# Optimization experiments

Measured on AMD Instinct MI355X. Metric: run time of the kernel, lower is better.

## Reference

```python
import jax, jax.numpy as jnp
import numpy as np

GRID_N = 3   # number of grid intervals (pykan 'grid')
K = 3        # spline order (pykan 'k')
IN_F = 512
OUT_F = 512
BATCH = 8
SEQ = 2048


def _extended_grid(d, dtype):
    # base grid: num+1 points over [-1, 1]; extend by K steps of h on each side (pykan extend_grid)
    pts = jnp.linspace(-1.0, 1.0, GRID_N + 1).astype(dtype)
    h = jnp.asarray(2.0 / GRID_N, dtype)
    left = pts[0] + h * jnp.arange(-K, 0, dtype=dtype)
    right = pts[-1] + h * jnp.arange(1, K + 1, dtype=dtype)
    ext = jnp.concatenate([left, pts, right])           # (GRID_N + 1 + 2K,)
    return jnp.broadcast_to(ext, (d, ext.shape[0]))     # per-input-feature grid (shared values)


def _bspline_basis(x, grid):
    # Cox-de Boor recursion, vectorized over tokens and input features.
    # x: (N, D), grid: (D, M) -> returns (N, D, M-1-K) = (N, D, GRID_N+K)
    x = x[:, :, None]                     # (N, D, 1)
    g = grid[None, :, :]                  # (1, D, M)
    B = ((x >= g[..., :-1]) & (x < g[..., 1:])).astype(x.dtype)
    for p in range(1, K + 1):
        left = (x - g[..., :-(p + 1)]) / (g[..., p:-1] - g[..., :-(p + 1)])
        right = (g[..., p + 1:] - x) / (g[..., p + 1:] - g[..., 1:-p])
        B = left * B[..., :-1] + right * B[..., 1:]
    return B


def setup_inputs() -> dict:
    key = jax.random.key(0)
    k1, k2, k3 = jax.random.split(key, 3)
    x = jax.random.normal(k1, (BATCH, SEQ, IN_F), dtype=jnp.float32)
    coef = jax.random.normal(k2, (OUT_F, IN_F, GRID_N + K), dtype=jnp.float32) * 0.1
    scale_base = (1.0 / np.sqrt(IN_F)) + (jax.random.uniform(k3, (OUT_F, IN_F), dtype=jnp.float32) * 2.0 - 1.0) * 0.1
    scale_sp = jnp.ones((OUT_F, IN_F), dtype=jnp.float32)
    bias = jnp.zeros((OUT_F,), dtype=jnp.float32)
    return {"x": x, "coef": coef, "scale_base": scale_base, "scale_sp": scale_sp, "bias": bias}


def reference(x, coef, scale_base, scale_sp, bias):
    B_, S, D = x.shape
    xf = x.reshape(-1, D)                               # (N, D) tokens
    grid = _extended_grid(D, xf.dtype)
    basis = _bspline_basis(xf, grid)                    # (N, D, GRID_N+K)
    base = jax.nn.silu(xf)                              # base activation per input feature
    # per-edge: scale_base*silu(x_i) + scale_sp*spline(x_i); sum over input features, add bias
    spline_w = scale_sp[..., None] * coef               # (O, D, GRID_N+K)
    y = (jnp.einsum('ni,oi->no', base, scale_base)
         + jnp.einsum('nib,oib->no', basis, spline_w)
         + bias[None, :])
    return y.reshape(B_, S, -1)
```

## Files before the change

kernel.cpp:

```cpp
#include <hip/hip_runtime.h>


typedef short        bf16x8 __attribute__((ext_vector_type(8)));
typedef float        f32x4  __attribute__((ext_vector_type(4)));
typedef unsigned int u32x4  __attribute__((ext_vector_type(4)));

#define NROWS 16384
#define DIN   512
#define DOUT  512
#define BM    64
#define BN    512
#define NKT   64

__device__ __forceinline__ unsigned short f2bf(float f) {
    unsigned int u = __float_as_uint(f);
    u += 0x7fffu + ((u >> 16) & 1u);
    return (unsigned short)(u >> 16);
}

__device__ __forceinline__ void kan_act_store(float xv, char* p16) {
    float S  = __builtin_fmaf(xv, 1.5f, 4.5f);
    float jf = floorf(S);
    float t  = S - jf;
    int   j  = (int)jf;
    float t2 = t * t;
    float t3 = t2 * t;
    float omt  = 1.0f - t;
    float omt2 = omt * omt;
    float n0 = omt2 * omt * (1.0f / 6.0f);
    float n1 = __builtin_fmaf(t3, 0.5f, -t2) + (2.0f / 3.0f);
    float u  = (t + t2) - t3;
    float n2 = __builtin_fmaf(u, 0.5f, 1.0f / 6.0f);
    float n3 = t3 * (1.0f / 6.0f);
    float e  = __expf(-xv);
    float si = xv * __builtin_amdgcn_rcpf(1.0f + e);

    unsigned P01, P23, WS;
    asm("v_cvt_pk_bf16_f32 %0, %1, %2" : "=v"(P01) : "v"(n0), "v"(n1));
    asm("v_cvt_pk_bf16_f32 %0, %1, %2" : "=v"(P23) : "v"(n2), "v"(n3));
    asm("v_cvt_pk_bf16_f32 %0, %1, %2" : "=v"(WS)  : "v"(si), "v"(0.0f));
    unsigned U = P01 << 16;
    unsigned V = (P01 >> 16) | (P23 << 16);
    unsigned Z = P23 >> 16;
    bool odd = (j & 1) != 0;
    unsigned c0 = odd ? U : P01;
    unsigned c1 = odd ? V : P23;
    unsigned c2 = odd ? Z : 0u;
    int b = (j - 2) >> 1;
    u32x4 w;
    w[0] = (b == 0) ? c0 : (b == -1) ? c1 : (b == -2) ? c2 : 0u;
    w[1] = (b == 1) ? c0 : (b ==  0) ? c1 : (b == -1) ? c2 : 0u;
    w[2] = (b == 2) ? c0 : (b ==  1) ? c1 : (b ==  0) ? c2 : 0u;
    w[3] = (b == 3) ? c0 : (b ==  2) ? c1 : (b ==  1) ? c2 : 0u;
    w[0] = (w[0] & 0xFFFF0000u) | (WS & 0xFFFFu);
    *(u32x4*)p16 = w;
}

__global__ __launch_bounds__(256) void kan_prep(
    const float* __restrict__ coef, const float* __restrict__ scale_base,
    const float* __restrict__ scale_sp, unsigned short* __restrict__ wt)
{
    int t = blockIdx.x * 256 + threadIdx.x;
    int o = t >> 9;
    int i = t & 511;
    float sb = scale_base[t];
    float sp = scale_sp[t];
    const float* cp = coef + (size_t)t * 6;
    bf16x8 w;
    w[0] = (short)f2bf(sb);
#pragma unroll
    for (int b = 0; b < 6; ++b) w[1 + b] = (short)f2bf(sp * cp[b]);
    w[7] = 0;
    int kt = i >> 3, s = i & 7, ks = s >> 2, fg = s & 3;
    size_t off = ((size_t)((kt * 2 + ks) * 512 + o)) * 64 + fg * 16;
    *(bf16x8*)((char*)wt + off) = w;
}

__global__ __launch_bounds__(512, 2) void kan_gemm(
    const float* __restrict__ x, const unsigned short* __restrict__ wt,
    const float* __restrict__ bias, float* __restrict__ y)
{
    __shared__ char As[2][BM * 128];

    const int tid  = threadIdx.x;
    const int lane = tid & 63;
    const int wid  = tid >> 6;

    int bid = blockIdx.x;
    int mt  = (bid & 7) * 32 + (bid >> 3);

    const int row0 = mt * BM;

    const int ar = tid >> 3;
    const int ap = tid & 7;
    const float* xp = x + (size_t)(row0 + ar) * DIN + ap;
    const int as_sw = (ar & 7) << 4;
    const int c0 = ap << 4;
    char* const arow0 = &As[0][ar * 128];
    char* const arow1 = &As[1][ar * 128];

    const int fr = lane & 15;
    const int fg = lane >> 4;

    const char* wb = (const char*)wt;
    int colpart[4];
#pragma unroll
    for (int n2 = 0; n2 < 4; ++n2)
        colpart[n2] = (wid * 64 + n2 * 16 + fr) * 64 + fg * 16;

#define LOADB(B, ktv)                                                         \
    {                                                                         \
        _Pragma("unroll")                                                     \
        for (int q = 0; q < 8; ++q) {                                         \
            int n2_ = q & 3, ks_ = q >> 2;                                    \
            B[q] = *(const bf16x8*)(wb + (size_t)((ktv) * 2 + ks_) * 32768    \
                                    + colpart[n2_]);                          \
        }                                                                     \
    }

    f32x4 acc[4][4];
#pragma unroll
    for (int m2 = 0; m2 < 4; ++m2)
#pragma unroll
        for (int n2 = 0; n2 < 4; ++n2) {
            f32x4 z = {0.f, 0.f, 0.f, 0.f};
            acc[m2][n2] = z;
        }

    bf16x8 Ba[8], Bb[8];

    LOADB(Ba, 0);
    kan_act_store(xp[0], arow0 + (c0 ^ as_sw));
    float xb = xp[8];
    asm volatile("s_waitcnt lgkmcnt(0)" ::: "memory");
    __builtin_amdgcn_s_barrier();

#define STEP(ktv, Bcur, Bnext)                                                \
    {                                                                         \
        const int cur_ = (ktv) & 1;                                           \
        bf16x8 af_[2][4];                                                     \
        _Pragma("unroll")                                                     \
        for (int ks_ = 0; ks_ < 2; ++ks_) {                                   \
            _Pragma("unroll")                                                 \
            for (int m2_ = 0; m2_ < 4; ++m2_) {                               \
                int rr_ = m2_ * 16 + fr;                                      \
                af_[ks_][m2_] = *(const bf16x8*)(&As[cur_][0] + rr_ * 128     \
                    + ((ks_ * 64 + fg * 16) ^ ((rr_ & 7) << 4)));             \
            }                                                                 \
        }                                                                     \
        if ((ktv) + 1 < NKT) {                                                \
            LOADB(Bnext, (ktv) + 1);                                          \
            char* rowp_ = (((ktv) + 1) & 1) ? arow1 : arow0;                  \
            kan_act_store(xb, rowp_ + (c0 ^ as_sw));                          \
            if ((ktv) + 2 < NKT) xb = xp[((ktv) + 2) * 8];                    \
        }                                                                     \
        __builtin_amdgcn_s_setprio(1);                                        \
        _Pragma("unroll")                                                     \
        for (int ks_ = 0; ks_ < 2; ++ks_)                                     \
            _Pragma("unroll")                                                 \
            for (int m2_ = 0; m2_ < 4; ++m2_)                                 \
                _Pragma("unroll")                                             \
                for (int n2_ = 0; n2_ < 4; ++n2_)                             \
                    acc[m2_][n2_] = __builtin_amdgcn_mfma_f32_16x16x32_bf16(  \
                        af_[ks_][m2_], Bcur[ks_ * 4 + n2_], acc[m2_][n2_],    \
                        0, 0, 0);                                             \
        __builtin_amdgcn_s_setprio(0);                                        \
        asm volatile("s_waitcnt lgkmcnt(0)" ::: "memory");                    \
        __builtin_amdgcn_s_barrier();                                         \
    }

    for (int kt = 0; kt < NKT; kt += 2) {
        STEP(kt, Ba, Bb);
        STEP(kt + 1, Bb, Ba);
    }

    const int orow0 = row0 + fg * 4;
    const int ocol0 = wid * 64 + fr;
#pragma unroll
    for (int n2 = 0; n2 < 4; ++n2) {
        float bv = bias[ocol0 + n2 * 16];
#pragma unroll
        for (int m2 = 0; m2 < 4; ++m2) {
#pragma unroll
            for (int r = 0; r < 4; ++r) {
                y[(size_t)(orow0 + m2 * 16 + r) * DOUT + (ocol0 + n2 * 16)]
                    = acc[m2][n2][r] + bv;
            }
        }
    }
#undef STEP
#undef LOADB
}

extern "C" void kernel_launch(void* const* d_in, const int* in_sizes, int n_in,
                              void* d_out, int out_size, void* d_ws, size_t ws_size,
                              hipStream_t stream)
{
    const float* x          = (const float*)d_in[0];
    const float* coef       = (const float*)d_in[1];
    const float* scale_base = (const float*)d_in[2];
    const float* scale_sp   = (const float*)d_in[3];
    const float* bias       = (const float*)d_in[4];
    unsigned short* wt = (unsigned short*)d_ws;
    float* y = (float*)d_out;

    kan_prep<<<1024, 256, 0, stream>>>(coef, scale_base, scale_sp, wt);
    kan_gemm<<<256, 512, 0, stream>>>(x, wt, bias, y);
}
```

Measured before the change: 91.01 us.

## Split GEMM block into MFMA consumer waves and activation producer waves

Adds four producer waves per block that compute the SiLU and cubic B-spline basis values and write them into the double-buffered LDS tile. The eight original waves now only load weights and issue MFMAs. The goal is to take the transcendental and basis arithmetic off the MFMA waves' critical path. In exchange the block grows to 768 threads with a tighter launch-bounds occupancy hint, which may restrict register allocation and cause spills of the accumulator tiles.

```diff
diff --git a/kernel.cpp b/kernel.cpp
--- a/kernel.cpp
+++ b/kernel.cpp
@@ -76,7 +76,7 @@
     *(bf16x8*)((char*)wt + off) = w;
 }
 
-__global__ __launch_bounds__(512, 2) void kan_gemm(
+__global__ __launch_bounds__(768, 3) void kan_gemm(
     const float* __restrict__ x, const unsigned short* __restrict__ wt,
     const float* __restrict__ bias, float* __restrict__ y)
 {
@@ -88,25 +88,17 @@
 
     int bid = blockIdx.x;
     int mt  = (bid & 7) * 32 + (bid >> 3);
-
     const int row0 = mt * BM;
-
-    const int ar = tid >> 3;
-    const int ap = tid & 7;
-    const float* xp = x + (size_t)(row0 + ar) * DIN + ap;
-    const int as_sw = (ar & 7) << 4;
-    const int c0 = ap << 4;
-    char* const arow0 = &As[0][ar * 128];
-    char* const arow1 = &As[1][ar * 128];
 
     const int fr = lane & 15;
     const int fg = lane >> 4;
 
-    const char* wb = (const char*)wt;
-    int colpart[4];
-#pragma unroll
-    for (int n2 = 0; n2 < 4; ++n2)
-        colpart[n2] = (wid * 64 + n2 * 16 + fr) * 64 + fg * 16;
+    if (wid < 8) {
+        const char* wb = (const char*)wt;
+        int colpart[4];
+#pragma unroll
+        for (int n2 = 0; n2 < 4; ++n2)
+            colpart[n2] = (wid * 64 + n2 * 16 + fr) * 64 + fg * 16;
 
 #define LOADB(B, ktv)                                                         \
     {                                                                         \
@@ -118,24 +110,20 @@
         }                                                                     \
     }
 
-    f32x4 acc[4][4];
-#pragma unroll
-    for (int m2 = 0; m2 < 4; ++m2)
-#pragma unroll
-        for (int n2 = 0; n2 < 4; ++n2) {
-            f32x4 z = {0.f, 0.f, 0.f, 0.f};
-            acc[m2][n2] = z;
-        }
-
-    bf16x8 Ba[8], Bb[8];
-
-    LOADB(Ba, 0);
-    kan_act_store(xp[0], arow0 + (c0 ^ as_sw));
-    float xb = xp[8];
-    asm volatile("s_waitcnt lgkmcnt(0)" ::: "memory");
-    __builtin_amdgcn_s_barrier();
-
-#define STEP(ktv, Bcur, Bnext)                                                \
+        f32x4 acc[4][4];
+#pragma unroll
+        for (int m2 = 0; m2 < 4; ++m2)
+#pragma unroll
+            for (int n2 = 0; n2 < 4; ++n2) {
+                f32x4 z = {0.f, 0.f, 0.f, 0.f};
+                acc[m2][n2] = z;
+            }
+
+        bf16x8 Ba[8], Bb[8];
+        LOADB(Ba, 0);
+        __builtin_amdgcn_s_barrier();
+
+#define CSTEP(ktv, Bcur, Bnext)                                               \
     {                                                                         \
         const int cur_ = (ktv) & 1;                                           \
         bf16x8 af_[2][4];                                                     \
@@ -148,13 +136,7 @@
                     + ((ks_ * 64 + fg * 16) ^ ((rr_ & 7) << 4)));             \
             }                                                                 \
         }                                                                     \
-        if ((ktv) + 1 < NKT) {                                                \
-            LOADB(Bnext, (ktv) + 1);                                          \
-            char* rowp_ = (((ktv) + 1) & 1) ? arow1 : arow0;                  \
-            kan_act_store(xb, rowp_ + (c0 ^ as_sw));                          \
-            if ((ktv) + 2 < NKT) xb = xp[((ktv) + 2) * 8];                    \
-        }                                                                     \
-        __builtin_amdgcn_s_setprio(1);                                        \
+        if ((ktv) + 1 < NKT) LOADB(Bnext, (ktv) + 1);                         \
         _Pragma("unroll")                                                     \
         for (int ks_ = 0; ks_ < 2; ++ks_)                                     \
             _Pragma("unroll")                                                 \
@@ -164,32 +146,62 @@
                     acc[m2_][n2_] = __builtin_amdgcn_mfma_f32_16x16x32_bf16(  \
                         af_[ks_][m2_], Bcur[ks_ * 4 + n2_], acc[m2_][n2_],    \
                         0, 0, 0);                                             \
-        __builtin_amdgcn_s_setprio(0);                                        \
         asm volatile("s_waitcnt lgkmcnt(0)" ::: "memory");                    \
         __builtin_amdgcn_s_barrier();                                         \
     }
 
-    for (int kt = 0; kt < NKT; kt += 2) {
-        STEP(kt, Ba, Bb);
-        STEP(kt + 1, Bb, Ba);
+        for (int kt = 0; kt < NKT; kt += 2) {
+            CSTEP(kt, Ba, Bb);
+            CSTEP(kt + 1, Bb, Ba);
+        }
+
+        const int orow0 = row0 + fg * 4;
+        const int ocol0 = wid * 64 + fr;
+#pragma unroll
+        for (int n2 = 0; n2 < 4; ++n2) {
+            float bv = bias[ocol0 + n2 * 16];
+#pragma unroll
+            for (int m2 = 0; m2 < 4; ++m2) {
+#pragma unroll
+                for (int r = 0; r < 4; ++r) {
+                    y[(size_t)(orow0 + m2 * 16 + r) * DOUT + (ocol0 + n2 * 16)]
+                        = acc[m2][n2][r] + bv;
+                }
+            }
+        }
+#undef CSTEP
+#undef LOADB
+    } else {
+        const int ptid = tid - 512;
+        const int ar = ptid >> 2;
+        const int ap = ptid & 3;
+        const float* xp = x + (size_t)(row0 + ar) * DIN + ap * 2;
+        const int as_sw = (ar & 7) << 4;
+        const int c0 = (ap * 2) << 4;
+        char* const arow0 = &As[0][ar * 128];
+        char* const arow1 = &As[1][ar * 128];
+
+        {
+            float2 xa = *(const float2*)(xp);
+            kan_act_store(xa.x, arow0 + (c0 ^ as_sw));
+            kan_act_store(xa.y, arow0 + ((c0 + 16) ^ as_sw));
+        }
+        float2 xb = *(const float2*)(xp + 8);
+        asm volatile("s_waitcnt lgkmcnt(0)" ::: "memory");
+        __builtin_amdgcn_s_barrier();
+
+        for (int kt = 0; kt < NKT; ++kt) {
+            if (kt + 1 < NKT) {
+                char* rowp = ((kt + 1) & 1) ? arow1 : arow0;
+                kan_act_store(xb.x, rowp + (c0 ^ as_sw));
+                kan_act_store(xb.y, rowp + ((c0 + 16) ^ as_sw));
+                if (kt + 2 < NKT)
+                    xb = *(const float2*)(xp + (kt + 2) * 8);
+            }
+            asm volatile("s_waitcnt lgkmcnt(0)" ::: "memory");
+            __builtin_amdgcn_s_barrier();
+        }
     }
-
-    const int orow0 = row0 + fg * 4;
-    const int ocol0 = wid * 64 + fr;
-#pragma unroll
-    for (int n2 = 0; n2 < 4; ++n2) {
-        float bv = bias[ocol0 + n2 * 16];
-#pragma unroll
-        for (int m2 = 0; m2 < 4; ++m2) {
-#pragma unroll
-            for (int r = 0; r < 4; ++r) {
-                y[(size_t)(orow0 + m2 * 16 + r) * DOUT + (ocol0 + n2 * 16)]
-                    = acc[m2][n2][r] + bv;
-            }
-        }
-    }
-#undef STEP
-#undef LOADB
 }
 
 extern "C" void kernel_launch(void* const* d_in, const int* in_sizes, int n_in,
@@ -205,5 +217,5 @@
     float* y = (float*)d_out;
 
     kan_prep<<<1024, 256, 0, stream>>>(coef, scale_base, scale_sp, wt);
-    kan_gemm<<<256, 512, 0, stream>>>(x, wt, bias, y);
-}
+    kan_gemm<<<256, 768, 0, stream>>>(x, wt, bias, y);
+}
```

Result: slower. 111.2 us (+22.1%).

## Deepen A-tile LDS pipeline to four stages and prefetch A fragments into registers

Applied to the files above, without the earlier changes.

Grows the LDS ring for the activation tile from two to four slots. The B-spline/SiLU activation is now produced two K-steps ahead, and A fragments for the next step are read from LDS into registers before the current step's MFMAs run. This is meant to hide LDS read latency and the activation compute behind the MFMA chain, and it also drops the setprio hints and skips the final barrier. In exchange it doubles LDS use and adds a second set of fragment registers, which at 2 blocks per CU with 512 threads may raise register pressure or cause spills.

```diff
diff --git a/kernel.cpp b/kernel.cpp
--- a/kernel.cpp
+++ b/kernel.cpp
@@ -80,7 +80,7 @@
     const float* __restrict__ x, const unsigned short* __restrict__ wt,
     const float* __restrict__ bias, float* __restrict__ y)
 {
-    __shared__ char As[2][BM * 128];
+    __shared__ char As[4][BM * 128];
 
     const int tid  = threadIdx.x;
     const int lane = tid & 63;
@@ -88,7 +88,6 @@
 
     int bid = blockIdx.x;
     int mt  = (bid & 7) * 32 + (bid >> 3);
-
     const int row0 = mt * BM;
 
     const int ar = tid >> 3;
@@ -96,8 +95,6 @@
     const float* xp = x + (size_t)(row0 + ar) * DIN + ap;
     const int as_sw = (ar & 7) << 4;
     const int c0 = ap << 4;
-    char* const arow0 = &As[0][ar * 128];
-    char* const arow1 = &As[1][ar * 128];
 
     const int fr = lane & 15;
     const int fg = lane >> 4;
@@ -118,6 +115,17 @@
         }                                                                     \
     }
 
+#define RD_AF(AF, slot)                                                       \
+    {                                                                         \
+        _Pragma("unroll")                                                     \
+        for (int q = 0; q < 8; ++q) {                                         \
+            int ks_ = q >> 2, m2_ = q & 3;                                    \
+            int rr_ = m2_ * 16 + fr;                                          \
+            AF[q] = *(const bf16x8*)(&As[slot][0] + rr_ * 128                 \
+                + ((ks_ * 64 + fg * 16) ^ ((rr_ & 7) << 4)));                 \
+        }                                                                     \
+    }
+
     f32x4 acc[4][4];
 #pragma unroll
     for (int m2 = 0; m2 < 4; ++m2)
@@ -128,33 +136,24 @@
         }
 
     bf16x8 Ba[8], Bb[8];
+    bf16x8 afA[8], afB[8];
 
     LOADB(Ba, 0);
-    kan_act_store(xp[0], arow0 + (c0 ^ as_sw));
-    float xb = xp[8];
+    kan_act_store(xp[0], &As[0][ar * 128] + (c0 ^ as_sw));
+    kan_act_store(xp[8], &As[1][ar * 128] + (c0 ^ as_sw));
+    float xb = xp[16];
     asm volatile("s_waitcnt lgkmcnt(0)" ::: "memory");
     __builtin_amdgcn_s_barrier();
-
-#define STEP(ktv, Bcur, Bnext)                                                \
+    RD_AF(afA, 0);
+
+#define STEP(ktv, Rn1, Rw, AFc, AFn, Bc, Bn)                                  \
     {                                                                         \
-        const int cur_ = (ktv) & 1;                                           \
-        bf16x8 af_[2][4];                                                     \
-        _Pragma("unroll")                                                     \
-        for (int ks_ = 0; ks_ < 2; ++ks_) {                                   \
-            _Pragma("unroll")                                                 \
-            for (int m2_ = 0; m2_ < 4; ++m2_) {                               \
-                int rr_ = m2_ * 16 + fr;                                      \
-                af_[ks_][m2_] = *(const bf16x8*)(&As[cur_][0] + rr_ * 128     \
-                    + ((ks_ * 64 + fg * 16) ^ ((rr_ & 7) << 4)));             \
-            }                                                                 \
-        }                                                                     \
-        if ((ktv) + 1 < NKT) {                                                \
-            LOADB(Bnext, (ktv) + 1);                                          \
-            char* rowp_ = (((ktv) + 1) & 1) ? arow1 : arow0;                  \
-            kan_act_store(xb, rowp_ + (c0 ^ as_sw));                          \
-            if ((ktv) + 2 < NKT) xb = xp[((ktv) + 2) * 8];                    \
-        }                                                                     \
-        __builtin_amdgcn_s_setprio(1);                                        \
+        if ((ktv) + 1 < NKT) LOADB(Bn, (ktv) + 1);                            \
+        if ((ktv) + 1 < NKT) RD_AF(AFn, Rn1);                                 \
+        if ((ktv) + 2 < NKT) {                                                \
+            kan_act_store(xb, &As[Rw][ar * 128] + (c0 ^ as_sw));              \
+            if ((ktv) + 3 < NKT) xb = xp[((ktv) + 3) * 8];                    \
+        }                                                                     \
         _Pragma("unroll")                                                     \
         for (int ks_ = 0; ks_ < 2; ++ks_)                                     \
             _Pragma("unroll")                                                 \
@@ -162,16 +161,19 @@
                 _Pragma("unroll")                                             \
                 for (int n2_ = 0; n2_ < 4; ++n2_)                             \
                     acc[m2_][n2_] = __builtin_amdgcn_mfma_f32_16x16x32_bf16(  \
-                        af_[ks_][m2_], Bcur[ks_ * 4 + n2_], acc[m2_][n2_],    \
+                        AFc[ks_ * 4 + m2_], Bc[ks_ * 4 + n2_], acc[m2_][n2_], \
                         0, 0, 0);                                             \
-        __builtin_amdgcn_s_setprio(0);                                        \
-        asm volatile("s_waitcnt lgkmcnt(0)" ::: "memory");                    \
-        __builtin_amdgcn_s_barrier();                                         \
-    }
-
-    for (int kt = 0; kt < NKT; kt += 2) {
-        STEP(kt, Ba, Bb);
-        STEP(kt + 1, Bb, Ba);
+        if ((ktv) + 1 < NKT) {                                                \
+            asm volatile("s_waitcnt lgkmcnt(0)" ::: "memory");                \
+            __builtin_amdgcn_s_barrier();                                     \
+        }                                                                     \
+    }
+
+    for (int kt = 0; kt < NKT; kt += 4) {
+        STEP(kt,     1, 2, afA, afB, Ba, Bb);
+        STEP(kt + 1, 2, 3, afB, afA, Bb, Ba);
+        STEP(kt + 2, 3, 0, afA, afB, Ba, Bb);
+        STEP(kt + 3, 0, 1, afB, afA, Bb, Ba);
     }
 
     const int orow0 = row0 + fg * 4;
@@ -189,6 +191,7 @@
         }
     }
 #undef STEP
+#undef RD_AF
 #undef LOADB
 }
 
```

After: 86.61 us. 4.8% less time.

## Hand-schedule GEMM main loop with inline-asm loads and explicit waitcnts

Applied to the files above, without the earlier changes.

Replaces compiler-generated global and LDS loads and stores in the KAN GEMM loop with inline assembly (global_load_dwordx4, ds_read_b128, ds_write_b128) and explicit s_waitcnt counters. The x value is now prefetched one step further ahead using two alternating registers. sched_barrier fences pin the order of loads, activation compute and MFMAs, and the setprio calls and the final barrier are removed. The aim is to overlap the next tile's memory traffic with the current MFMAs and to avoid conservative compiler waits. The cost is fragile manual vmcnt/lgkmcnt accounting that can race if the counts are wrong.

```diff
diff --git a/kernel.cpp b/kernel.cpp
--- a/kernel.cpp
+++ b/kernel.cpp
@@ -18,7 +18,7 @@
     return (unsigned short)(u >> 16);
 }
 
-__device__ __forceinline__ void kan_act_store(float xv, char* p16) {
+__device__ __forceinline__ u32x4 kan_act(float xv) {
     float S  = __builtin_fmaf(xv, 1.5f, 4.5f);
     float jf = floorf(S);
     float t  = S - jf;
@@ -53,7 +53,7 @@
     w[2] = (b == 2) ? c0 : (b ==  1) ? c1 : (b ==  0) ? c2 : 0u;
     w[3] = (b == 3) ? c0 : (b ==  2) ? c1 : (b ==  1) ? c2 : 0u;
     w[0] = (w[0] & 0xFFFF0000u) | (WS & 0xFFFFu);
-    *(u32x4*)p16 = w;
+    return w;
 }
 
 __global__ __launch_bounds__(256) void kan_prep(
@@ -88,7 +88,6 @@
 
     int bid = blockIdx.x;
     int mt  = (bid & 7) * 32 + (bid >> 3);
-
     const int row0 = mt * BM;
 
     const int ar = tid >> 3;
@@ -96,27 +95,17 @@
     const float* xp = x + (size_t)(row0 + ar) * DIN + ap;
     const int as_sw = (ar & 7) << 4;
     const int c0 = ap << 4;
-    char* const arow0 = &As[0][ar * 128];
-    char* const arow1 = &As[1][ar * 128];
 
     const int fr = lane & 15;
     const int fg = lane >> 4;
 
-    const char* wb = (const char*)wt;
-    int colpart[4];
+    const unsigned asb =
+        (unsigned)(unsigned long long)(__attribute__((address_space(3))) char*)&As[0][0];
+
+    const char* pB[4];
 #pragma unroll
     for (int n2 = 0; n2 < 4; ++n2)
-        colpart[n2] = (wid * 64 + n2 * 16 + fr) * 64 + fg * 16;
-
-#define LOADB(B, ktv)                                                         \
-    {                                                                         \
-        _Pragma("unroll")                                                     \
-        for (int q = 0; q < 8; ++q) {                                         \
-            int n2_ = q & 3, ks_ = q >> 2;                                    \
-            B[q] = *(const bf16x8*)(wb + (size_t)((ktv) * 2 + ks_) * 32768    \
-                                    + colpart[n2_]);                          \
-        }                                                                     \
-    }
+        pB[n2] = (const char*)wt + (size_t)((wid * 64 + n2 * 16 + fr) * 64 + fg * 16);
 
     f32x4 acc[4][4];
 #pragma unroll
@@ -128,33 +117,65 @@
         }
 
     bf16x8 Ba[8], Bb[8];
-
-    LOADB(Ba, 0);
-    kan_act_store(xp[0], arow0 + (c0 ^ as_sw));
-    float xb = xp[8];
-    asm volatile("s_waitcnt lgkmcnt(0)" ::: "memory");
+    float  xA, xB;
+
+    {
+        float x0 = xp[0];
+        u32x4 w0 = kan_act(x0);
+        unsigned woff = asb + ar * 128 + (c0 ^ as_sw);
+        asm volatile("ds_write_b128 %0, %1" :: "v"(woff), "v"(w0));
+    }
+#pragma unroll
+    for (int q = 0; q < 8; ++q) {
+        int n2_ = q & 3, ks_ = q >> 2;
+        const void* a_ = pB[n2_] + ks_ * 32768;
+        asm volatile("global_load_dwordx4 %0, %1, off" : "=&v"(Ba[q]) : "v"(a_));
+    }
+    asm volatile("global_load_dword %0, %1, off"
+                 : "=&v"(xA) : "v"((const void*)(xp + 8)));
+    asm volatile("s_waitcnt lgkmcnt(0)");
     __builtin_amdgcn_s_barrier();
 
-#define STEP(ktv, Bcur, Bnext)                                                \
+#define STEP(ktv, Bc, Bn, xcur, xnext)                                        \
     {                                                                         \
         const int cur_ = (ktv) & 1;                                           \
-        bf16x8 af_[2][4];                                                     \
+        const unsigned abase_ = asb + cur_ * 8192;                            \
+        bf16x8 AF[8];                                                         \
         _Pragma("unroll")                                                     \
-        for (int ks_ = 0; ks_ < 2; ++ks_) {                                   \
+        for (int q = 0; q < 8; ++q) {                                         \
+            int ks_ = q >> 2, m2_ = q & 3;                                    \
+            int rr_ = m2_ * 16 + fr;                                          \
+            unsigned off_ = abase_ + rr_ * 128                                \
+                + ((unsigned)(ks_ * 64 + fg * 16) ^ (unsigned)((rr_ & 7) << 4)); \
+            asm volatile("ds_read_b128 %0, %1" : "=&v"(AF[q]) : "v"(off_));   \
+        }                                                                     \
+        const bool hn_ = (ktv) + 1 < NKT;                                     \
+        if (hn_) {                                                            \
+            size_t ko_ = (size_t)((ktv) + 1) * 65536;                         \
             _Pragma("unroll")                                                 \
-            for (int m2_ = 0; m2_ < 4; ++m2_) {                               \
-                int rr_ = m2_ * 16 + fr;                                      \
-                af_[ks_][m2_] = *(const bf16x8*)(&As[cur_][0] + rr_ * 128     \
-                    + ((ks_ * 64 + fg * 16) ^ ((rr_ & 7) << 4)));             \
+            for (int q = 0; q < 8; ++q) {                                     \
+                int n2_ = q & 3, ks_ = q >> 2;                                \
+                const void* a_ = pB[n2_] + ko_ + ks_ * 32768;                 \
+                asm volatile("global_load_dwordx4 %0, %1, off"                \
+                             : "=&v"(Bn[q]) : "v"(a_));                       \
             }                                                                 \
-        }                                                                     \
-        if ((ktv) + 1 < NKT) {                                                \
-            LOADB(Bnext, (ktv) + 1);                                          \
-            char* rowp_ = (((ktv) + 1) & 1) ? arow1 : arow0;                  \
-            kan_act_store(xb, rowp_ + (c0 ^ as_sw));                          \
-            if ((ktv) + 2 < NKT) xb = xp[((ktv) + 2) * 8];                    \
-        }                                                                     \
-        __builtin_amdgcn_s_setprio(1);                                        \
+            int xo_ = ((ktv) + 2 < NKT) ? ((ktv) + 2) * 8 : 0;                \
+            asm volatile("global_load_dword %0, %1, off"                      \
+                         : "=&v"(xnext) : "v"((const void*)(xp + xo_)));      \
+            asm volatile("s_waitcnt vmcnt(9)");                               \
+        } else {                                                              \
+            asm volatile("s_waitcnt vmcnt(0)");                               \
+        }                                                                     \
+        __builtin_amdgcn_sched_barrier(0);                                    \
+        if (hn_) {                                                            \
+            u32x4 w_ = kan_act(xcur);                                         \
+            unsigned woff_ = asb + (cur_ ^ 1) * 8192 + ar * 128 + (c0 ^ as_sw); \
+            asm volatile("ds_write_b128 %0, %1" :: "v"(woff_), "v"(w_));      \
+            asm volatile("s_waitcnt lgkmcnt(1)");                             \
+        } else {                                                              \
+            asm volatile("s_waitcnt lgkmcnt(0)");                             \
+        }                                                                     \
+        __builtin_amdgcn_sched_barrier(0);                                    \
         _Pragma("unroll")                                                     \
         for (int ks_ = 0; ks_ < 2; ++ks_)                                     \
             _Pragma("unroll")                                                 \
@@ -162,16 +183,17 @@
                 _Pragma("unroll")                                             \
                 for (int n2_ = 0; n2_ < 4; ++n2_)                             \
                     acc[m2_][n2_] = __builtin_amdgcn_mfma_f32_16x16x32_bf16(  \
-                        af_[ks_][m2_], Bcur[ks_ * 4 + n2_], acc[m2_][n2_],    \
+                        AF[ks_ * 4 + m2_], Bc[ks_ * 4 + n2_], acc[m2_][n2_],  \
                         0, 0, 0);                                             \
-        __builtin_amdgcn_s_setprio(0);                                        \
-        asm volatile("s_waitcnt lgkmcnt(0)" ::: "memory");                    \
-        __builtin_amdgcn_s_barrier();                                         \
+        if (hn_) {                                                            \
+            asm volatile("s_waitcnt lgkmcnt(0)");                             \
+            __builtin_amdgcn_s_barrier();                                     \
+        }                                                                     \
     }
 
     for (int kt = 0; kt < NKT; kt += 2) {
-        STEP(kt, Ba, Bb);
-        STEP(kt + 1, Bb, Ba);
+        STEP(kt,     Ba, Bb, xA, xB);
+        STEP(kt + 1, Bb, Ba, xB, xA);
     }
 
     const int orow0 = row0 + fg * 4;
@@ -189,7 +211,6 @@
         }
     }
 #undef STEP
-#undef LOADB
 }
 
 extern "C" void kernel_launch(void* const* d_in, const int* in_sizes, int n_in,
```

Measured after the change: 78.88 us. 13.3% less time.
